# Performance work log

Hardware: AMD Instinct MI355X
Metric: run time of the kernel (lower is better)

Reference implementation:

```python
import jax, jax.numpy as jnp
import numpy as np
from jax import lax

K = 20  # number of propagation steps (init kwarg k)


def _conv(x, w, padding):
    return lax.conv_general_dilated(
        x, w, window_strides=(1, 1), padding=padding,
        dimension_numbers=('NCHW', 'OIHW', 'NCHW'))


def _max_pool3(v):
    # 3x3 max pool, stride 1, SAME padding (pad value -inf like torch MaxPool2d)
    return lax.reduce_window(v, -jnp.inf, lax.max,
                             (1, 1, 3, 3), (1, 1, 1, 1), 'SAME')


def setup_inputs() -> dict:
    key = jax.random.key(0)
    k1, k2, k3, k4 = jax.random.split(key, 4)
    B, H, W = 16, 256, 256
    image = jax.random.uniform(k1, (B, 2, H, W), dtype=jnp.float32)
    # conv params, kaiming-ish scale
    W_h = jax.random.normal(k2, (150, 1, 3, 3), dtype=jnp.float32) * (1.0 / 3.0)
    b_h = jax.random.normal(k3, (150,), dtype=jnp.float32) * 0.1
    W_p = jax.random.normal(k4, (1, 150, 1, 1), dtype=jnp.float32) * (1.0 / np.sqrt(150.0))
    return {"image": image, "W_h": W_h, "b_h": b_h, "W_p": W_p}


def reference(image, W_h, b_h, W_p):
    occ = image[:, 0:1, :, :]  # [B,1,H,W] occupancy / free-space channel
    r = image[:, 1:2, :, :]    # [B,1,H,W] reward channel

    h = jax.nn.relu(_conv(occ, W_h, 'SAME') + b_h[None, :, None, None])  # [B,150,H,W]
    p = jax.nn.sigmoid(_conv(h, W_p, 'VALID'))                            # [B,1,H,W]

    def step(v, _):
        v = jnp.maximum(v, r + p * (_max_pool3(v) - r))
        return v, None

    v, _ = lax.scan(step, r, None, length=K)
    v = jnp.where(occ > 0.49, v, -jnp.ones_like(v))
    return v
```

## Files before the change

kernel.cpp:

```cpp
#include <hip/hip_runtime.h>
#include <hip/hip_bf16.h>
#include <math.h>


#define SENT -1e30f

typedef short short8 __attribute__((ext_vector_type(8)));
typedef float f32x16 __attribute__((ext_vector_type(16)));

__device__ __forceinline__ uint32_t pkbf(float lo, float hi) {
    uint32_t r;
    asm("v_cvt_pk_bf16_f32 %0, %1, %2" : "=v"(r) : "v"(lo), "v"(hi));
    return r;
}

__device__ __forceinline__ uint32_t bfu(float f) {
    __hip_bfloat16 h = __float2bfloat16(f);
    ushort u; __builtin_memcpy(&u, &h, 2);
    return (uint32_t)u;
}

__global__ void pack_a_kernel(const float* __restrict__ Wh,
                              const float* __restrict__ bh,
                              uint4* __restrict__ wsA)
{
    const int lane = threadIdx.x;
    const int half = lane >> 5;
    const int col0 = lane & 31;
#pragma unroll
    for (int g = 0; g < 5; ++g) {
        int ch = 32 * g + col0;
        bool ok = ch < 150;
        int cs = ok ? ch : 0;
        float w0 = ok ? Wh[cs*9+0] : 0.f, w1 = ok ? Wh[cs*9+1] : 0.f;
        float w2 = ok ? Wh[cs*9+2] : 0.f, w3 = ok ? Wh[cs*9+3] : 0.f;
        float w4 = ok ? Wh[cs*9+4] : 0.f, w5 = ok ? Wh[cs*9+5] : 0.f;
        float w6 = ok ? Wh[cs*9+6] : 0.f, w7 = ok ? Wh[cs*9+7] : 0.f;
        float w8 = ok ? Wh[cs*9+8] : 0.f, bb = ok ? bh[cs]     : 0.f;
        uint4 q;
        if (half) {
            q.x = (bfu(bb) << 16) | bfu(w8);
            q.y = 0; q.z = 0; q.w = 0;
        } else {
            q.x = (bfu(w1) << 16) | bfu(w0);
            q.y = (bfu(w3) << 16) | bfu(w2);
            q.z = (bfu(w5) << 16) | bfu(w4);
            q.w = (bfu(w7) << 16) | bfu(w6);
        }
        wsA[g * 64 + lane] = q;
    }
}

__global__ __launch_bounds__(256, 4) void conv_p_mfma(
    const float* __restrict__ image, const float* __restrict__ Wp,
    const uint4* __restrict__ wsA, float* __restrict__ pout)
{
    const int tid  = threadIdx.x;
    const int wv   = tid >> 6;
    const int lane = tid & 63;
    const int half = lane >> 5;
    const int col0 = lane & 31;
    const int b    = blockIdx.z;
    const int y    = blockIdx.y * 4 + wv;
    const int x0   = blockIdx.x * 32;
    const float* occ = image + (size_t)b * 131072;

    uint4 q0 = wsA[0 * 64 + lane];
    uint4 q1 = wsA[1 * 64 + lane];
    uint4 q2 = wsA[2 * 64 + lane];
    uint4 q3 = wsA[3 * 64 + lane];
    uint4 q4 = wsA[4 * 64 + lane];

    int cc = x0 - 1 + lane;
    bool cok = (lane < 34) & (cc >= 0) & (cc < 256);
    float r0 = (cok & (y >= 1))   ? occ[(y - 1) * 256 + cc] : 0.f;
    float r1 = cok                ? occ[y * 256 + cc]       : 0.f;
    float r2 = (cok & (y <= 254)) ? occ[(y + 1) * 256 + cc] : 0.f;

    __shared__ __align__(16) float lds_wp[160];
    if (tid < 160) lds_wp[tid] = (tid < 150) ? Wp[tid] : 0.f;
    __syncthreads();

    float t0 = __shfl(r0, col0), t1 = __shfl(r0, col0 + 1), t2 = __shfl(r0, col0 + 2);
    float t3 = __shfl(r1, col0), t4 = __shfl(r1, col0 + 1), t5 = __shfl(r1, col0 + 2);
    float t6 = __shfl(r2, col0), t7 = __shfl(r2, col0 + 1), t8 = __shfl(r2, col0 + 2);

    union { uint32_t u[4]; short8 s; } bb;
    bb.u[0] = half ? pkbf(t8, 1.0f) : pkbf(t0, t1);
    bb.u[1] = half ? 0u : pkbf(t2, t3);
    bb.u[2] = half ? 0u : pkbf(t4, t5);
    bb.u[3] = half ? 0u : pkbf(t6, t7);
    short8 bfr = bb.s;

    union { uint4 q; short8 s; } ua0, ua1, ua2, ua3, ua4;
    ua0.q = q0; ua1.q = q1; ua2.q = q2; ua3.q = q3; ua4.q = q4;

    const f32x16 kZero = {};
    f32x16 d0 = __builtin_amdgcn_mfma_f32_32x32x16_bf16(ua0.s, bfr, kZero, 0, 0, 0);
    f32x16 d1 = __builtin_amdgcn_mfma_f32_32x32x16_bf16(ua1.s, bfr, kZero, 0, 0, 0);
    f32x16 d2 = __builtin_amdgcn_mfma_f32_32x32x16_bf16(ua2.s, bfr, kZero, 0, 0, 0);
    f32x16 d3 = __builtin_amdgcn_mfma_f32_32x32x16_bf16(ua3.s, bfr, kZero, 0, 0, 0);
    f32x16 d4 = __builtin_amdgcn_mfma_f32_32x32x16_bf16(ua4.s, bfr, kZero, 0, 0, 0);

    float s0 = 0.f, s1 = 0.f, s2 = 0.f, s3 = 0.f;
#define RED(D, G)                                                            \
    {                                                                        \
        const float4 wA = *(const float4*)&lds_wp[32 * (G) + 0  + 4 * half]; \
        const float4 wB = *(const float4*)&lds_wp[32 * (G) + 8  + 4 * half]; \
        const float4 wC = *(const float4*)&lds_wp[32 * (G) + 16 + 4 * half]; \
        const float4 wD = *(const float4*)&lds_wp[32 * (G) + 24 + 4 * half]; \
        s0 = fmaf(wA.x, fmaxf(D[0],  0.f), s0);                              \
        s1 = fmaf(wA.y, fmaxf(D[1],  0.f), s1);                              \
        s2 = fmaf(wA.z, fmaxf(D[2],  0.f), s2);                              \
        s3 = fmaf(wA.w, fmaxf(D[3],  0.f), s3);                              \
        s0 = fmaf(wB.x, fmaxf(D[4],  0.f), s0);                              \
        s1 = fmaf(wB.y, fmaxf(D[5],  0.f), s1);                              \
        s2 = fmaf(wB.z, fmaxf(D[6],  0.f), s2);                              \
        s3 = fmaf(wB.w, fmaxf(D[7],  0.f), s3);                              \
        s0 = fmaf(wC.x, fmaxf(D[8],  0.f), s0);                              \
        s1 = fmaf(wC.y, fmaxf(D[9],  0.f), s1);                              \
        s2 = fmaf(wC.z, fmaxf(D[10], 0.f), s2);                              \
        s3 = fmaf(wC.w, fmaxf(D[11], 0.f), s3);                              \
        s0 = fmaf(wD.x, fmaxf(D[12], 0.f), s0);                              \
        s1 = fmaf(wD.y, fmaxf(D[13], 0.f), s1);                              \
        s2 = fmaf(wD.z, fmaxf(D[14], 0.f), s2);                              \
        s3 = fmaf(wD.w, fmaxf(D[15], 0.f), s3);                              \
    }
    RED(d0, 0) RED(d1, 1) RED(d2, 2) RED(d3, 3) RED(d4, 4)
#undef RED

    float s = (s0 + s1) + (s2 + s3);
    s += __shfl_xor(s, 32);

    float p = 1.f / (1.f + __expf(-s));
    if (lane < 32)
        pout[(size_t)b * 65536 + y * 256 + x0 + lane] = p;
}

__global__ __launch_bounds__(512, 2) void mvprop_kernel(
    const float* __restrict__ image, const float* __restrict__ pbuf,
    float* __restrict__ out)
{
    const int tid  = threadIdx.x;
    const int w    = tid >> 6;
    const int lane = tid & 63;
    const int b    = blockIdx.z;
    const int gy0  = blockIdx.y * 16 - 20;
    const int x4   = lane * 4;

    const float* rimg = image + (size_t)b * 131072 + 65536;
    const float* pp   = pbuf  + (size_t)b * 65536;

    float v[7][4], r[7][4], p[7][4];
#pragma unroll
    for (int i = 0; i < 7; ++i) {
        int gy = gy0 + w * 7 + i;
        if (gy >= 0 && gy < 256) {
            float4 rv = *(const float4*)&rimg[gy * 256 + x4];
            float4 pv = *(const float4*)&pp[gy * 256 + x4];
            r[i][0] = rv.x; r[i][1] = rv.y; r[i][2] = rv.z; r[i][3] = rv.w;
            p[i][0] = pv.x; p[i][1] = pv.y; p[i][2] = pv.z; p[i][3] = pv.w;
        } else {
            r[i][0] = r[i][1] = r[i][2] = r[i][3] = SENT;
            p[i][0] = p[i][1] = p[i][2] = p[i][3] = 0.f;
        }
        v[i][0] = r[i][0]; v[i][1] = r[i][1];
        v[i][2] = r[i][2]; v[i][3] = r[i][3];
    }

    __shared__ float4 gT[2][8][64];
    __shared__ float4 gB[2][8][64];

    for (int t = 0; t < 20; ++t) {
        int bf = t & 1;
        gT[bf][w][lane] = make_float4(v[0][0], v[0][1], v[0][2], v[0][3]);
        gB[bf][w][lane] = make_float4(v[6][0], v[6][1], v[6][2], v[6][3]);
        __syncthreads();
        float4 abv = (w > 0) ? gB[bf][w - 1][lane]
                             : make_float4(SENT, SENT, SENT, SENT);
        float4 blw = (w < 7) ? gT[bf][w + 1][lane]
                             : make_float4(SENT, SENT, SENT, SENT);

        float pv0 = abv.x, pv1 = abv.y, pv2 = abv.z, pv3 = abv.w;
#pragma unroll
        for (int i = 0; i < 7; ++i) {
            float c0 = v[i][0], c1 = v[i][1], c2 = v[i][2], c3 = v[i][3];
            float n0, n1, n2, n3;
            if (i < 6) { n0 = v[i+1][0]; n1 = v[i+1][1]; n2 = v[i+1][2]; n3 = v[i+1][3]; }
            else       { n0 = blw.x;     n1 = blw.y;     n2 = blw.z;     n3 = blw.w;     }
            float vm0 = fmaxf(pv0, fmaxf(c0, n0));
            float vm1 = fmaxf(pv1, fmaxf(c1, n1));
            float vm2 = fmaxf(pv2, fmaxf(c2, n2));
            float vm3 = fmaxf(pv3, fmaxf(c3, n3));
            float lL = __shfl_up(vm3, 1);
            lL = (lane == 0) ? SENT : lL;
            float rR = __shfl_down(vm0, 1);
            rR = (lane == 63) ? SENT : rR;
            float h0 = fmaxf(lL,  fmaxf(vm0, vm1));
            float h1 = fmaxf(vm0, fmaxf(vm1, vm2));
            float h2 = fmaxf(vm1, fmaxf(vm2, vm3));
            float h3 = fmaxf(vm2, fmaxf(vm3, rR));
            v[i][0] = fmaxf(c0, fmaf(p[i][0], h0 - r[i][0], r[i][0]));
            v[i][1] = fmaxf(c1, fmaf(p[i][1], h1 - r[i][1], r[i][1]));
            v[i][2] = fmaxf(c2, fmaf(p[i][2], h2 - r[i][2], r[i][2]));
            v[i][3] = fmaxf(c3, fmaf(p[i][3], h3 - r[i][3], r[i][3]));
            pv0 = c0; pv1 = c1; pv2 = c2; pv3 = c3;
        }
    }

    const float* occ = image + (size_t)b * 131072;
#pragma unroll
    for (int i = 0; i < 7; ++i) {
        int e = w * 7 + i;
        if (e >= 20 && e < 36) {
            int gy = gy0 + e;
            float4 ov = *(const float4*)&occ[gy * 256 + x4];
            float4 o;
            o.x = (ov.x > 0.49f) ? v[i][0] : -1.f;
            o.y = (ov.y > 0.49f) ? v[i][1] : -1.f;
            o.z = (ov.z > 0.49f) ? v[i][2] : -1.f;
            o.w = (ov.w > 0.49f) ? v[i][3] : -1.f;
            *(float4*)&out[(size_t)b * 65536 + gy * 256 + x4] = o;
        }
    }
}

extern "C" void kernel_launch(void* const* d_in, const int* in_sizes, int n_in,
                              void* d_out, int out_size, void* d_ws, size_t ws_size,
                              hipStream_t stream) {
    const float* image = (const float*)d_in[0];
    const float* Wh    = (const float*)d_in[1];
    const float* bh    = (const float*)d_in[2];
    const float* Wp    = (const float*)d_in[3];
    float* out  = (float*)d_out;
    float* pbuf = (float*)d_ws;
    uint4* wsA  = (uint4*)((char*)d_ws + (4 << 20));

    pack_a_kernel<<<1, 64, 0, stream>>>(Wh, bh, wsA);
    conv_p_mfma<<<dim3(8, 64, 16), dim3(256), 0, stream>>>(image, Wp, wsA, pbuf);
    mvprop_kernel<<<dim3(1, 16, 16), dim3(512), 0, stream>>>(image, pbuf, out);
}
```

Baseline: 53.43 us.

## Fold 1x1 conv weights into 3x3 filters, sorting channels by sign

The pack kernel multiplies each 3x3 filter and bias by its 1x1 output weight and reorders the channels so that positive-weight channels come first, padded to groups of 32. This uses relu(x)*w = max(wx,0) for w>=0 and min(wx,0) for w<0, so the conv kernel drops the per-element FMA with Wp and only sums max or min. The conv kernel also stages the packed weights in LDS and loads its 3x3 neighbourhood directly from global memory instead of shuffling. It may now issue six MFMAs instead of five, and there is a uniform branch per group.

```diff
diff --git a/kernel.cpp b/kernel.cpp
--- a/kernel.cpp
+++ b/kernel.cpp
@@ -22,38 +22,61 @@
 
 __global__ void pack_a_kernel(const float* __restrict__ Wh,
                               const float* __restrict__ bh,
+                              const float* __restrict__ Wp,
                               uint4* __restrict__ wsA)
 {
-    const int lane = threadIdx.x;
-    const int half = lane >> 5;
-    const int col0 = lane & 31;
-#pragma unroll
-    for (int g = 0; g < 5; ++g) {
-        int ch = 32 * g + col0;
-        bool ok = ch < 150;
-        int cs = ok ? ch : 0;
-        float w0 = ok ? Wh[cs*9+0] : 0.f, w1 = ok ? Wh[cs*9+1] : 0.f;
-        float w2 = ok ? Wh[cs*9+2] : 0.f, w3 = ok ? Wh[cs*9+3] : 0.f;
-        float w4 = ok ? Wh[cs*9+4] : 0.f, w5 = ok ? Wh[cs*9+5] : 0.f;
-        float w6 = ok ? Wh[cs*9+6] : 0.f, w7 = ok ? Wh[cs*9+7] : 0.f;
-        float w8 = ok ? Wh[cs*9+8] : 0.f, bb = ok ? bh[cs]     : 0.f;
+    __shared__ int scan[256];
+    const int tid = threadIdx.x;
+    const bool valid = tid < 150;
+    float wp = valid ? Wp[tid] : 0.f;
+    bool pos = valid && (wp >= 0.f);
+    bool neg = valid && (wp < 0.f);
+
+    int v = (pos ? 1 : 0) | ((neg ? 1 : 0) << 16);
+    scan[tid] = v;
+    __syncthreads();
+    for (int off = 1; off < 256; off <<= 1) {
+        int x = scan[tid];
+        int y = (tid >= off) ? scan[tid - off] : 0;
+        __syncthreads();
+        scan[tid] = x + y;
+        __syncthreads();
+    }
+    int incl  = scan[tid];
+    int total = scan[255];
+    int P     = total & 0xffff;
+    int rankPos = (incl & 0xffff) - (pos ? 1 : 0);
+    int rankNeg = (incl >> 16)    - (neg ? 1 : 0);
+    int Ppad  = (P + 31) & ~31;
+    int nPosG = Ppad >> 5;
+    int newidx = pos ? rankPos : (Ppad + rankNeg);
+
+    if (tid < 384) wsA[tid] = make_uint4(0u, 0u, 0u, 0u);
+    if (tid == 0)  ((uint32_t*)(wsA + 384))[0] = (uint32_t)nPosG;
+    __syncthreads();
+
+    if (valid) {
+        float s  = wp;
+        float w0 = Wh[tid*9+0]*s, w1 = Wh[tid*9+1]*s, w2 = Wh[tid*9+2]*s;
+        float w3 = Wh[tid*9+3]*s, w4 = Wh[tid*9+4]*s, w5 = Wh[tid*9+5]*s;
+        float w6 = Wh[tid*9+6]*s, w7 = Wh[tid*9+7]*s, w8 = Wh[tid*9+8]*s;
+        float bb = bh[tid]*s;
+        int g = newidx >> 5, col0 = newidx & 31;
         uint4 q;
-        if (half) {
-            q.x = (bfu(bb) << 16) | bfu(w8);
-            q.y = 0; q.z = 0; q.w = 0;
-        } else {
-            q.x = (bfu(w1) << 16) | bfu(w0);
-            q.y = (bfu(w3) << 16) | bfu(w2);
-            q.z = (bfu(w5) << 16) | bfu(w4);
-            q.w = (bfu(w7) << 16) | bfu(w6);
-        }
-        wsA[g * 64 + lane] = q;
+        q.x = (bfu(w1) << 16) | bfu(w0);
+        q.y = (bfu(w3) << 16) | bfu(w2);
+        q.z = (bfu(w5) << 16) | bfu(w4);
+        q.w = (bfu(w7) << 16) | bfu(w6);
+        wsA[g * 64 + col0] = q;
+        q.x = (bfu(bb) << 16) | bfu(w8);
+        q.y = 0; q.z = 0; q.w = 0;
+        wsA[g * 64 + 32 + col0] = q;
     }
 }
 
 __global__ __launch_bounds__(256, 4) void conv_p_mfma(
-    const float* __restrict__ image, const float* __restrict__ Wp,
-    const uint4* __restrict__ wsA, float* __restrict__ pout)
+    const float* __restrict__ image, const uint4* __restrict__ wsA,
+    float* __restrict__ pout)
 {
     const int tid  = threadIdx.x;
     const int wv   = tid >> 6;
@@ -62,28 +85,33 @@
     const int col0 = lane & 31;
     const int b    = blockIdx.z;
     const int y    = blockIdx.y * 4 + wv;
-    const int x0   = blockIdx.x * 32;
+    const int px   = blockIdx.x * 32 + col0;
     const float* occ = image + (size_t)b * 131072;
 
-    uint4 q0 = wsA[0 * 64 + lane];
-    uint4 q1 = wsA[1 * 64 + lane];
-    uint4 q2 = wsA[2 * 64 + lane];
-    uint4 q3 = wsA[3 * 64 + lane];
-    uint4 q4 = wsA[4 * 64 + lane];
-
-    int cc = x0 - 1 + lane;
-    bool cok = (lane < 34) & (cc >= 0) & (cc < 256);
-    float r0 = (cok & (y >= 1))   ? occ[(y - 1) * 256 + cc] : 0.f;
-    float r1 = cok                ? occ[y * 256 + cc]       : 0.f;
-    float r2 = (cok & (y <= 254)) ? occ[(y + 1) * 256 + cc] : 0.f;
-
-    __shared__ __align__(16) float lds_wp[160];
-    if (tid < 160) lds_wp[tid] = (tid < 150) ? Wp[tid] : 0.f;
+    __shared__ __align__(16) uint4 lds_a[384];
+    lds_a[tid] = wsA[tid];
+    if (tid < 128) lds_a[256 + tid] = wsA[256 + tid];
+    uint32_t nPosG = __builtin_amdgcn_readfirstlane(((const uint32_t*)(wsA + 384))[0]);
+
+    float t0, t1, t2, t3, t4, t5, t6, t7, t8;
+    {
+        bool x0ok = (px >= 1), x2ok = (px <= 254);
+        int xm = px - 1, xp = px + 1;
+        bool y0ok = (y >= 1), y2ok = (y <= 254);
+        const float* rm = occ + (y - 1) * 256;
+        const float* rc = occ + y * 256;
+        const float* rp = occ + (y + 1) * 256;
+        t0 = (y0ok & x0ok) ? rm[xm] : 0.f;
+        t1 =  y0ok         ? rm[px] : 0.f;
+        t2 = (y0ok & x2ok) ? rm[xp] : 0.f;
+        t3 =  x0ok         ? rc[xm] : 0.f;
+        t4 =                 rc[px];
+        t5 =  x2ok         ? rc[xp] : 0.f;
+        t6 = (y2ok & x0ok) ? rp[xm] : 0.f;
+        t7 =  y2ok         ? rp[px] : 0.f;
+        t8 = (y2ok & x2ok) ? rp[xp] : 0.f;
+    }
     __syncthreads();
-
-    float t0 = __shfl(r0, col0), t1 = __shfl(r0, col0 + 1), t2 = __shfl(r0, col0 + 2);
-    float t3 = __shfl(r1, col0), t4 = __shfl(r1, col0 + 1), t5 = __shfl(r1, col0 + 2);
-    float t6 = __shfl(r2, col0), t7 = __shfl(r2, col0 + 1), t8 = __shfl(r2, col0 + 2);
 
     union { uint32_t u[4]; short8 s; } bb;
     bb.u[0] = half ? pkbf(t8, 1.0f) : pkbf(t0, t1);
@@ -92,49 +120,38 @@
     bb.u[3] = half ? 0u : pkbf(t6, t7);
     short8 bfr = bb.s;
 
-    union { uint4 q; short8 s; } ua0, ua1, ua2, ua3, ua4;
-    ua0.q = q0; ua1.q = q1; ua2.q = q2; ua3.q = q3; ua4.q = q4;
-
     const f32x16 kZero = {};
-    f32x16 d0 = __builtin_amdgcn_mfma_f32_32x32x16_bf16(ua0.s, bfr, kZero, 0, 0, 0);
-    f32x16 d1 = __builtin_amdgcn_mfma_f32_32x32x16_bf16(ua1.s, bfr, kZero, 0, 0, 0);
-    f32x16 d2 = __builtin_amdgcn_mfma_f32_32x32x16_bf16(ua2.s, bfr, kZero, 0, 0, 0);
-    f32x16 d3 = __builtin_amdgcn_mfma_f32_32x32x16_bf16(ua3.s, bfr, kZero, 0, 0, 0);
-    f32x16 d4 = __builtin_amdgcn_mfma_f32_32x32x16_bf16(ua4.s, bfr, kZero, 0, 0, 0);
-
-    float s0 = 0.f, s1 = 0.f, s2 = 0.f, s3 = 0.f;
-#define RED(D, G)                                                            \
-    {                                                                        \
-        const float4 wA = *(const float4*)&lds_wp[32 * (G) + 0  + 4 * half]; \
-        const float4 wB = *(const float4*)&lds_wp[32 * (G) + 8  + 4 * half]; \
-        const float4 wC = *(const float4*)&lds_wp[32 * (G) + 16 + 4 * half]; \
-        const float4 wD = *(const float4*)&lds_wp[32 * (G) + 24 + 4 * half]; \
-        s0 = fmaf(wA.x, fmaxf(D[0],  0.f), s0);                              \
-        s1 = fmaf(wA.y, fmaxf(D[1],  0.f), s1);                              \
-        s2 = fmaf(wA.z, fmaxf(D[2],  0.f), s2);                              \
-        s3 = fmaf(wA.w, fmaxf(D[3],  0.f), s3);                              \
-        s0 = fmaf(wB.x, fmaxf(D[4],  0.f), s0);                              \
-        s1 = fmaf(wB.y, fmaxf(D[5],  0.f), s1);                              \
-        s2 = fmaf(wB.z, fmaxf(D[6],  0.f), s2);                              \
-        s3 = fmaf(wB.w, fmaxf(D[7],  0.f), s3);                              \
-        s0 = fmaf(wC.x, fmaxf(D[8],  0.f), s0);                              \
-        s1 = fmaf(wC.y, fmaxf(D[9],  0.f), s1);                              \
-        s2 = fmaf(wC.z, fmaxf(D[10], 0.f), s2);                              \
-        s3 = fmaf(wC.w, fmaxf(D[11], 0.f), s3);                              \
-        s0 = fmaf(wD.x, fmaxf(D[12], 0.f), s0);                              \
-        s1 = fmaf(wD.y, fmaxf(D[13], 0.f), s1);                              \
-        s2 = fmaf(wD.z, fmaxf(D[14], 0.f), s2);                              \
-        s3 = fmaf(wD.w, fmaxf(D[15], 0.f), s3);                              \
-    }
-    RED(d0, 0) RED(d1, 1) RED(d2, 2) RED(d3, 3) RED(d4, 4)
-#undef RED
-
-    float s = (s0 + s1) + (s2 + s3);
+    float S0 = 0.f, S1 = 0.f, S2 = 0.f, S3 = 0.f;
+#pragma unroll
+    for (uint32_t g = 0; g < 6; ++g) {
+        union { uint4 q; short8 s; } ua;
+        ua.q = lds_a[g * 64 + lane];
+        f32x16 d = __builtin_amdgcn_mfma_f32_32x32x16_bf16(ua.s, bfr, kZero, 0, 0, 0);
+        if (g < nPosG) {
+#pragma unroll
+            for (int q = 0; q < 4; ++q) {
+                S0 += fmaxf(d[q*4+0], 0.f);
+                S1 += fmaxf(d[q*4+1], 0.f);
+                S2 += fmaxf(d[q*4+2], 0.f);
+                S3 += fmaxf(d[q*4+3], 0.f);
+            }
+        } else {
+#pragma unroll
+            for (int q = 0; q < 4; ++q) {
+                S0 += fminf(d[q*4+0], 0.f);
+                S1 += fminf(d[q*4+1], 0.f);
+                S2 += fminf(d[q*4+2], 0.f);
+                S3 += fminf(d[q*4+3], 0.f);
+            }
+        }
+    }
+
+    float s = (S0 + S1) + (S2 + S3);
     s += __shfl_xor(s, 32);
 
     float p = 1.f / (1.f + __expf(-s));
-    if (lane < 32)
-        pout[(size_t)b * 65536 + y * 256 + x0 + lane] = p;
+    if (!half)
+        pout[(size_t)b * 65536 + y * 256 + px] = p;
 }
 
 __global__ __launch_bounds__(512, 2) void mvprop_kernel(
@@ -236,7 +253,7 @@
     float* pbuf = (float*)d_ws;
     uint4* wsA  = (uint4*)((char*)d_ws + (4 << 20));
 
-    pack_a_kernel<<<1, 64, 0, stream>>>(Wh, bh, wsA);
-    conv_p_mfma<<<dim3(8, 64, 16), dim3(256), 0, stream>>>(image, Wp, wsA, pbuf);
+    pack_a_kernel<<<1, 256, 0, stream>>>(Wh, bh, Wp, wsA);
+    conv_p_mfma<<<dim3(8, 64, 16), dim3(256), 0, stream>>>(image, wsA, pbuf);
     mvprop_kernel<<<dim3(1, 16, 16), dim3(512), 0, stream>>>(image, pbuf, out);
 }
```

Measured after the change: 56.00 us. +4.8%, slower.
